# Optimization experiments

Hardware: AMD Instinct MI355X
Metric: run time of the kernel (lower is better)

The kernel has to match this reference:

```python
import jax, jax.numpy as jnp
import numpy as np


def setup_inputs() -> dict:
    key = jax.random.key(0)
    k1, k2, k3, k4 = jax.random.split(key, 4)
    B, T, C = 4, 1024, 768
    H, D = 12, 64
    scale = 0.02  # typical init scale for stability
    return {
        "x": jax.random.normal(k1, (B, T, C), dtype=jnp.float32),
        "Wq": jax.random.normal(k2, (H, C, D), dtype=jnp.float32) * scale,
        "Wk": jax.random.normal(k3, (H, C, D), dtype=jnp.float32) * scale,
        "Wv": jax.random.normal(k4, (H, C, D), dtype=jnp.float32) * scale,
    }


def reference(x, Wq, Wk, Wv):
    # x: [B,T,C]; Wq/Wk/Wv: [H,C,D]
    B, T, C = x.shape
    H, _, D = Wq.shape
    q = jnp.einsum("btc,hcd->bhtd", x, Wq)
    k = jnp.einsum("btc,hcd->bhtd", x, Wk)
    v = jnp.einsum("btc,hcd->bhtd", x, Wv)
    scores = jnp.einsum("bhtd,bhsd->bhts", q, k) * (D ** -0.5)
    causal = jnp.tril(jnp.ones((T, T), dtype=bool))
    scores = jnp.where(causal, scores, jnp.finfo(scores.dtype).min)
    attn = jax.nn.softmax(scores, axis=-1)
    out = jnp.einsum("bhts,bhsd->bhtd", attn, v)  # [B,H,T,D]
    # concat heads along last dim: [B,T,H*D]
    return out.transpose(0, 2, 1, 3).reshape(B, T, H * D)
```

## Files before the change

kernel.cpp:

```cpp
#include <hip/hip_runtime.h>
#include <math.h>
#include <stdint.h>

constexpr int B_ = 4, T_ = 1024, C_ = 768, H_ = 12, D_ = 64;
constexpr int BH_ = B_ * H_;
constexpr int M_ = B_ * T_;
constexpr int N_ = 3 * H_ * D_;

using f32x4 = __attribute__((ext_vector_type(4))) float;
using s16x8 = __attribute__((ext_vector_type(8))) short;

__device__ __forceinline__ unsigned short f2bf(float f) {
    union { float f; uint32_t u; } v; v.f = f;
    uint32_t u = v.u + 0x7fffu + ((v.u >> 16) & 1u);
    return (unsigned short)(u >> 16);
}

__global__ __launch_bounds__(256) void cast_x_kernel(
    const float* __restrict__ x, unsigned short* __restrict__ X16)
{
    int i = blockIdx.x * 256 + threadIdx.x;
    float4 v = ((const float4*)x)[i];
    ushort4 o;
    o.x = f2bf(v.x); o.y = f2bf(v.y); o.z = f2bf(v.z); o.w = f2bf(v.w);
    ((ushort4*)X16)[i] = o;
}

__global__ __launch_bounds__(256) void cast_w_kernel(
    const float* __restrict__ Wq, const float* __restrict__ Wk,
    const float* __restrict__ Wv, unsigned short* __restrict__ Wt)
{
    __shared__ unsigned short L[64][72];
    const int hp = blockIdx.x / 12, ct = blockIdx.x % 12;
    const int p = hp / H_, h = hp % H_;
    const float* W = (p == 0 ? Wq : (p == 1 ? Wk : Wv)) + (size_t)h * C_ * D_ + (size_t)ct * 64 * D_;
    const int tid = threadIdx.x;
#pragma unroll
    for (int it = 0; it < 4; ++it) {
        int f = tid + it * 256;
        int c = f >> 4, dg = f & 15;
        float4 v = ((const float4*)(W + (size_t)c * D_))[dg];
        L[dg * 4 + 0][c] = f2bf(v.x);
        L[dg * 4 + 1][c] = f2bf(v.y);
        L[dg * 4 + 2][c] = f2bf(v.z);
        L[dg * 4 + 3][c] = f2bf(v.w);
    }
    __syncthreads();
#pragma unroll
    for (int it = 0; it < 2; ++it) {
        int f = tid + it * 256;
        int d = f >> 3, cg = f & 7;
        uint4 v = *(const uint4*)&L[d][cg * 8];
        *(uint4*)(Wt + (size_t)(hp * 64 + d) * C_ + ct * 64 + cg * 8) = v;
    }
}

__global__ __launch_bounds__(256) void proj_kernel(
    const unsigned short* __restrict__ X16,
    const unsigned short* __restrict__ Wt,
    unsigned short* __restrict__ Qp,
    unsigned short* __restrict__ Kp,
    unsigned short* __restrict__ Vt)
{
    __shared__ unsigned short As[128 * 32];
    __shared__ unsigned short Bs[128 * 32];
    const int tid = threadIdx.x;
    const int l = tid & 63, w = tid >> 6;
    const int n0 = blockIdx.x * 128, m0 = blockIdx.y * 128;
    const int msub = (w >> 1) * 64, nsub = (w & 1) * 64;
    const int lr = l & 15, lg = l >> 4;

    f32x4 acc[4][4];
#pragma unroll
    for (int i = 0; i < 4; ++i)
#pragma unroll
        for (int j = 0; j < 4; ++j)
            acc[i][j] = (f32x4){0.f, 0.f, 0.f, 0.f};

    for (int k0 = 0; k0 < C_; k0 += 32) {
#pragma unroll
        for (int it = 0; it < 2; ++it) {
            int f = tid + it * 256;
            int m = f >> 2, kc = f & 3;
            uint4 va = *(const uint4*)(X16 + (size_t)(m0 + m) * C_ + k0 + kc * 8);
            *(uint4*)(As + f * 8) = va;
            uint4 vb = *(const uint4*)(Wt + (size_t)(n0 + m) * C_ + k0 + kc * 8);
            *(uint4*)(Bs + f * 8) = vb;
        }
        __syncthreads();
        s16x8 a[4], b[4];
#pragma unroll
        for (int i = 0; i < 4; ++i) {
            a[i] = *(const s16x8*)(As + (msub + i * 16 + lr) * 32 + lg * 8);
            b[i] = *(const s16x8*)(Bs + (nsub + i * 16 + lr) * 32 + lg * 8);
        }
#pragma unroll
        for (int i = 0; i < 4; ++i)
#pragma unroll
            for (int j = 0; j < 4; ++j)
                acc[i][j] = __builtin_amdgcn_mfma_f32_16x16x32_bf16(a[i], b[j], acc[i][j], 0, 0, 0);
        __syncthreads();
    }

    const int bq = m0 >> 10;
#pragma unroll
    for (int j = 0; j < 4; ++j) {
        int n = n0 + nsub + j * 16 + lr;
        int hp = n >> 6, d = n & 63;
        int p = hp / H_, hh = hp % H_;
        int bh = bq * H_ + hh;
#pragma unroll
        for (int i = 0; i < 4; ++i) {
            int tb = m0 + msub + i * 16 + lg * 4;
            int t = tb & (T_ - 1);
            if (p == 2) {
                ushort4 pv;
                pv.x = f2bf(acc[i][j][0]); pv.y = f2bf(acc[i][j][1]);
                pv.z = f2bf(acc[i][j][2]); pv.w = f2bf(acc[i][j][3]);
                *(ushort4*)(Vt + ((size_t)bh * D_ + d) * T_ + t) = pv;
            } else {
                unsigned short* P = (p == 0 ? Qp : Kp) + (size_t)bh * T_ * D_ + d;
#pragma unroll
                for (int r = 0; r < 4; ++r)
                    P[(size_t)(t + r) * D_] = f2bf(acc[i][j][r]);
            }
        }
    }
}

__global__ __launch_bounds__(64) void attn_kernel(
    const unsigned short* __restrict__ Qp,
    const unsigned short* __restrict__ Kp,
    const unsigned short* __restrict__ Vt,
    float* __restrict__ out)
{
    __shared__ unsigned short Pl[16 * 72];
    const int l = threadIdx.x;
    const int lr = l & 15, lg = l >> 4;
    const int bh = blockIdx.x >> 5, pr = blockIdx.x & 31;
    const int bq = bh / H_, hh = bh % H_;
    const unsigned short* Q = Qp + (size_t)bh * T_ * D_;
    const unsigned short* K = Kp + (size_t)bh * T_ * D_;
    const unsigned short* V = Vt + (size_t)bh * D_ * T_;
    float* O = out + (size_t)bq * T_ * (H_ * D_) + hh * D_;

    const float NEG = -30000.0f;

    for (int half = 0; half < 2; ++half) {
        const int qi = half ? (63 - pr) : pr;
        const int q0 = qi * 16;
        s16x8 qa0 = *(const s16x8*)(Q + (size_t)(q0 + lr) * D_ + lg * 8);
        s16x8 qa1 = *(const s16x8*)(Q + (size_t)(q0 + lr) * D_ + 32 + lg * 8);

        f32x4 o[4];
        float m[4], ll[4];
#pragma unroll
        for (int g = 0; g < 4; ++g) o[g] = (f32x4){0.f, 0.f, 0.f, 0.f};
#pragma unroll
        for (int r = 0; r < 4; ++r) { m[r] = NEG; ll[r] = 0.f; }

        const int ntile = (qi >> 2) + 1;
        for (int j = 0; j < ntile; ++j) {
            const int kv0 = j * 64;
            f32x4 s[4];
#pragma unroll
            for (int g = 0; g < 4; ++g) s[g] = (f32x4){0.f, 0.f, 0.f, 0.f};
#pragma unroll
            for (int g = 0; g < 4; ++g) {
                const unsigned short* kr = K + (size_t)(kv0 + g * 16 + lr) * D_ + lg * 8;
                s16x8 kb0 = *(const s16x8*)(kr);
                s16x8 kb1 = *(const s16x8*)(kr + 32);
                s[g] = __builtin_amdgcn_mfma_f32_16x16x32_bf16(qa0, kb0, s[g], 0, 0, 0);
                s[g] = __builtin_amdgcn_mfma_f32_16x16x32_bf16(qa1, kb1, s[g], 0, 0, 0);
            }
            const bool last = (j == ntile - 1);
            const float sc = 0.125f;
#pragma unroll
            for (int g = 0; g < 4; ++g)
#pragma unroll
                for (int r = 0; r < 4; ++r) {
                    float v = s[g][r] * sc;
                    if (last && (kv0 + g * 16 + lr > q0 + lg * 4 + r)) v = NEG;
                    s[g][r] = v;
                }
#pragma unroll
            for (int r = 0; r < 4; ++r) {
                float mx = fmaxf(fmaxf(s[0][r], s[1][r]), fmaxf(s[2][r], s[3][r]));
                mx = fmaxf(mx, __shfl_xor(mx, 1));
                mx = fmaxf(mx, __shfl_xor(mx, 2));
                mx = fmaxf(mx, __shfl_xor(mx, 4));
                mx = fmaxf(mx, __shfl_xor(mx, 8));
                float mn = fmaxf(m[r], mx);
                float corr = __expf(m[r] - mn);
                float p[4], rs = 0.f;
#pragma unroll
                for (int g = 0; g < 4; ++g) { p[g] = __expf(s[g][r] - mn); rs += p[g]; }
                rs += __shfl_xor(rs, 1); rs += __shfl_xor(rs, 2);
                rs += __shfl_xor(rs, 4); rs += __shfl_xor(rs, 8);
                ll[r] = ll[r] * corr + rs;
                m[r] = mn;
#pragma unroll
                for (int g = 0; g < 4; ++g) {
                    o[g][r] *= corr;
                    Pl[(lg * 4 + r) * 72 + g * 16 + lr] = f2bf(p[g]);
                }
            }
            __syncthreads();

            s16x8 pa0 = *(const s16x8*)(Pl + lr * 72 + lg * 8);
            s16x8 pa1 = *(const s16x8*)(Pl + lr * 72 + 32 + lg * 8);
#pragma unroll
            for (int g = 0; g < 4; ++g) {
                const unsigned short* vr = V + (size_t)(g * 16 + lr) * T_ + kv0 + lg * 8;
                s16x8 vb0 = *(const s16x8*)(vr);
                s16x8 vb1 = *(const s16x8*)(vr + 32);
                o[g] = __builtin_amdgcn_mfma_f32_16x16x32_bf16(pa0, vb0, o[g], 0, 0, 0);
                o[g] = __builtin_amdgcn_mfma_f32_16x16x32_bf16(pa1, vb1, o[g], 0, 0, 0);
            }
            __syncthreads();
        }
        float rinv[4];
#pragma unroll
        for (int r = 0; r < 4; ++r) rinv[r] = 1.0f / ll[r];
#pragma unroll
        for (int g = 0; g < 4; ++g)
#pragma unroll
            for (int r = 0; r < 4; ++r)
                O[(size_t)(q0 + lg * 4 + r) * (H_ * D_) + g * 16 + lr] = o[g][r] * rinv[r];
    }
}

extern "C" void kernel_launch(void* const* d_in, const int* in_sizes, int n_in,
                              void* d_out, int out_size, void* d_ws, size_t ws_size,
                              hipStream_t stream) {
    const float* x  = (const float*)d_in[0];
    const float* Wq = (const float*)d_in[1];
    const float* Wk = (const float*)d_in[2];
    const float* Wv = (const float*)d_in[3];
    float* out = (float*)d_out;

    char* ws = (char*)d_ws;
    unsigned short* X16 = (unsigned short*)(ws);
    unsigned short* Wt  = (unsigned short*)(ws + 6291456);
    unsigned short* Qp  = (unsigned short*)(ws + 9830400);
    unsigned short* Kp  = (unsigned short*)(ws + 16121856);
    unsigned short* Vt  = (unsigned short*)(ws + 22413312);

    cast_x_kernel<<<(M_ * C_ / 4) / 256, 256, 0, stream>>>(x, X16);
    cast_w_kernel<<<36 * 12, 256, 0, stream>>>(Wq, Wk, Wv, Wt);
    proj_kernel<<<dim3(N_ / 128, M_ / 128), 256, 0, stream>>>(X16, Wt, Qp, Kp, Vt);
    attn_kernel<<<BH_ * 32, 64, 0, stream>>>(Qp, Kp, Vt, out);
}
```

Measured before the change: 183.4 us.

## Split attention blocks per query tile, map heads to XCDs, prefetch K and V

Each attention block now handles a single 16-row query tile instead of a balanced pair, doubling the grid to 3072 single-wave blocks. Block indices are remapped so that all query tiles of one batch-head land on the same XCD, which should improve L2 reuse of K and V. V tiles are loaded together with K before the QK MFMAs, hiding V latency behind the softmax. A launch-bounds occupancy hint is added. The change gives up the paired load balancing, so causal work per block is now uneven, and holding 16 extra vector registers for K and V may limit occupancy.

```diff
diff --git a/kernel.cpp b/kernel.cpp
--- a/kernel.cpp
+++ b/kernel.cpp
@@ -128,7 +128,7 @@
     }
 }
 
-__global__ __launch_bounds__(64) void attn_kernel(
+__global__ __launch_bounds__(64, 3) void attn_kernel(
     const unsigned short* __restrict__ Qp,
     const unsigned short* __restrict__ Kp,
     const unsigned short* __restrict__ Vt,
@@ -137,7 +137,10 @@
     __shared__ unsigned short Pl[16 * 72];
     const int l = threadIdx.x;
     const int lr = l & 15, lg = l >> 4;
-    const int bh = blockIdx.x >> 5, pr = blockIdx.x & 31;
+    const int id = blockIdx.x;
+    const int xcd = id & 7, rest = id >> 3;
+    const int qi = rest & 63;
+    const int bh = xcd + 8 * (rest >> 6);
     const int bq = bh / H_, hh = bh % H_;
     const unsigned short* Q = Qp + (size_t)bh * T_ * D_;
     const unsigned short* K = Kp + (size_t)bh * T_ * D_;
@@ -145,89 +148,94 @@
     float* O = out + (size_t)bq * T_ * (H_ * D_) + hh * D_;
 
     const float NEG = -30000.0f;
-
-    for (int half = 0; half < 2; ++half) {
-        const int qi = half ? (63 - pr) : pr;
-        const int q0 = qi * 16;
-        s16x8 qa0 = *(const s16x8*)(Q + (size_t)(q0 + lr) * D_ + lg * 8);
-        s16x8 qa1 = *(const s16x8*)(Q + (size_t)(q0 + lr) * D_ + 32 + lg * 8);
-
-        f32x4 o[4];
-        float m[4], ll[4];
-#pragma unroll
-        for (int g = 0; g < 4; ++g) o[g] = (f32x4){0.f, 0.f, 0.f, 0.f};
-#pragma unroll
-        for (int r = 0; r < 4; ++r) { m[r] = NEG; ll[r] = 0.f; }
-
-        const int ntile = (qi >> 2) + 1;
-        for (int j = 0; j < ntile; ++j) {
-            const int kv0 = j * 64;
-            f32x4 s[4];
-#pragma unroll
-            for (int g = 0; g < 4; ++g) s[g] = (f32x4){0.f, 0.f, 0.f, 0.f};
+    const int q0 = qi * 16;
+
+    s16x8 qa0 = *(const s16x8*)(Q + (size_t)(q0 + lr) * D_ + lg * 8);
+    s16x8 qa1 = *(const s16x8*)(Q + (size_t)(q0 + lr) * D_ + 32 + lg * 8);
+
+    f32x4 o[4];
+    float m[4], ll[4];
+#pragma unroll
+    for (int g = 0; g < 4; ++g) o[g] = (f32x4){0.f, 0.f, 0.f, 0.f};
+#pragma unroll
+    for (int r = 0; r < 4; ++r) { m[r] = NEG; ll[r] = 0.f; }
+
+    const int ntile = (qi >> 2) + 1;
+    for (int j = 0; j < ntile; ++j) {
+        const int kv0 = j * 64;
+        s16x8 kb[8], vb[8];
+#pragma unroll
+        for (int g = 0; g < 4; ++g) {
+            const unsigned short* kr = K + (size_t)(kv0 + g * 16 + lr) * D_ + lg * 8;
+            kb[2 * g]     = *(const s16x8*)(kr);
+            kb[2 * g + 1] = *(const s16x8*)(kr + 32);
+        }
+#pragma unroll
+        for (int g = 0; g < 4; ++g) {
+            const unsigned short* vr = V + (size_t)(g * 16 + lr) * T_ + kv0 + lg * 8;
+            vb[2 * g]     = *(const s16x8*)(vr);
+            vb[2 * g + 1] = *(const s16x8*)(vr + 32);
+        }
+        f32x4 s[4];
+#pragma unroll
+        for (int g = 0; g < 4; ++g) s[g] = (f32x4){0.f, 0.f, 0.f, 0.f};
+#pragma unroll
+        for (int g = 0; g < 4; ++g) {
+            s[g] = __builtin_amdgcn_mfma_f32_16x16x32_bf16(qa0, kb[2 * g],     s[g], 0, 0, 0);
+            s[g] = __builtin_amdgcn_mfma_f32_16x16x32_bf16(qa1, kb[2 * g + 1], s[g], 0, 0, 0);
+        }
+        const bool last = (j == ntile - 1);
+        const float sc = 0.125f;
+#pragma unroll
+        for (int g = 0; g < 4; ++g)
+#pragma unroll
+            for (int r = 0; r < 4; ++r) {
+                float v = s[g][r] * sc;
+                if (last && (kv0 + g * 16 + lr > q0 + lg * 4 + r)) v = NEG;
+                s[g][r] = v;
+            }
+#pragma unroll
+        for (int r = 0; r < 4; ++r) {
+            float mx = fmaxf(fmaxf(s[0][r], s[1][r]), fmaxf(s[2][r], s[3][r]));
+            mx = fmaxf(mx, __shfl_xor(mx, 1));
+            mx = fmaxf(mx, __shfl_xor(mx, 2));
+            mx = fmaxf(mx, __shfl_xor(mx, 4));
+            mx = fmaxf(mx, __shfl_xor(mx, 8));
+            float mn = fmaxf(m[r], mx);
+            float corr = __expf(m[r] - mn);
+            float p[4], rs = 0.f;
+#pragma unroll
+            for (int g = 0; g < 4; ++g) { p[g] = __expf(s[g][r] - mn); rs += p[g]; }
+            rs += __shfl_xor(rs, 1); rs += __shfl_xor(rs, 2);
+            rs += __shfl_xor(rs, 4); rs += __shfl_xor(rs, 8);
+            ll[r] = ll[r] * corr + rs;
+            m[r] = mn;
 #pragma unroll
             for (int g = 0; g < 4; ++g) {
-                const unsigned short* kr = K + (size_t)(kv0 + g * 16 + lr) * D_ + lg * 8;
-                s16x8 kb0 = *(const s16x8*)(kr);
-                s16x8 kb1 = *(const s16x8*)(kr + 32);
-                s[g] = __builtin_amdgcn_mfma_f32_16x16x32_bf16(qa0, kb0, s[g], 0, 0, 0);
-                s[g] = __builtin_amdgcn_mfma_f32_16x16x32_bf16(qa1, kb1, s[g], 0, 0, 0);
+                o[g][r] *= corr;
+                Pl[(lg * 4 + r) * 72 + g * 16 + lr] = f2bf(p[g]);
             }
-            const bool last = (j == ntile - 1);
-            const float sc = 0.125f;
-#pragma unroll
-            for (int g = 0; g < 4; ++g)
-#pragma unroll
-                for (int r = 0; r < 4; ++r) {
-                    float v = s[g][r] * sc;
-                    if (last && (kv0 + g * 16 + lr > q0 + lg * 4 + r)) v = NEG;
-                    s[g][r] = v;
-                }
-#pragma unroll
-            for (int r = 0; r < 4; ++r) {
-                float mx = fmaxf(fmaxf(s[0][r], s[1][r]), fmaxf(s[2][r], s[3][r]));
-                mx = fmaxf(mx, __shfl_xor(mx, 1));
-                mx = fmaxf(mx, __shfl_xor(mx, 2));
-                mx = fmaxf(mx, __shfl_xor(mx, 4));
-                mx = fmaxf(mx, __shfl_xor(mx, 8));
-                float mn = fmaxf(m[r], mx);
-                float corr = __expf(m[r] - mn);
-                float p[4], rs = 0.f;
-#pragma unroll
-                for (int g = 0; g < 4; ++g) { p[g] = __expf(s[g][r] - mn); rs += p[g]; }
-                rs += __shfl_xor(rs, 1); rs += __shfl_xor(rs, 2);
-                rs += __shfl_xor(rs, 4); rs += __shfl_xor(rs, 8);
-                ll[r] = ll[r] * corr + rs;
-                m[r] = mn;
-#pragma unroll
-                for (int g = 0; g < 4; ++g) {
-                    o[g][r] *= corr;
-                    Pl[(lg * 4 + r) * 72 + g * 16 + lr] = f2bf(p[g]);
-                }
-            }
-            __syncthreads();
-
-            s16x8 pa0 = *(const s16x8*)(Pl + lr * 72 + lg * 8);
-            s16x8 pa1 = *(const s16x8*)(Pl + lr * 72 + 32 + lg * 8);
-#pragma unroll
-            for (int g = 0; g < 4; ++g) {
-                const unsigned short* vr = V + (size_t)(g * 16 + lr) * T_ + kv0 + lg * 8;
-                s16x8 vb0 = *(const s16x8*)(vr);
-                s16x8 vb1 = *(const s16x8*)(vr + 32);
-                o[g] = __builtin_amdgcn_mfma_f32_16x16x32_bf16(pa0, vb0, o[g], 0, 0, 0);
-                o[g] = __builtin_amdgcn_mfma_f32_16x16x32_bf16(pa1, vb1, o[g], 0, 0, 0);
-            }
-            __syncthreads();
-        }
-        float rinv[4];
-#pragma unroll
-        for (int r = 0; r < 4; ++r) rinv[r] = 1.0f / ll[r];
-#pragma unroll
-        for (int g = 0; g < 4; ++g)
-#pragma unroll
-            for (int r = 0; r < 4; ++r)
-                O[(size_t)(q0 + lg * 4 + r) * (H_ * D_) + g * 16 + lr] = o[g][r] * rinv[r];
-    }
+        }
+        __syncthreads();
+
+        s16x8 pa0 = *(const s16x8*)(Pl + lr * 72 + lg * 8);
+        s16x8 pa1 = *(const s16x8*)(Pl + lr * 72 + 32 + lg * 8);
+#pragma unroll
+        for (int g = 0; g < 4; ++g) {
+            o[g] = __builtin_amdgcn_mfma_f32_16x16x32_bf16(pa0, vb[2 * g],     o[g], 0, 0, 0);
+            o[g] = __builtin_amdgcn_mfma_f32_16x16x32_bf16(pa1, vb[2 * g + 1], o[g], 0, 0, 0);
+        }
+        __syncthreads();
+    }
+
+    float rinv[4];
+#pragma unroll
+    for (int r = 0; r < 4; ++r) rinv[r] = 1.0f / ll[r];
+#pragma unroll
+    for (int g = 0; g < 4; ++g)
+#pragma unroll
+        for (int r = 0; r < 4; ++r)
+            O[(size_t)(q0 + lg * 4 + r) * (H_ * D_) + g * 16 + lr] = o[g][r] * rinv[r];
 }
 
 extern "C" void kernel_launch(void* const* d_in, const int* in_sizes, int n_in,
@@ -249,5 +257,5 @@
     cast_x_kernel<<<(M_ * C_ / 4) / 256, 256, 0, stream>>>(x, X16);
     cast_w_kernel<<<36 * 12, 256, 0, stream>>>(Wq, Wk, Wv, Wt);
     proj_kernel<<<dim3(N_ / 128, M_ / 128), 256, 0, stream>>>(X16, Wt, Qp, Kp, Vt);
-    attn_kernel<<<BH_ * 32, 64, 0, stream>>>(Qp, Kp, Vt, out);
-}
+    attn_kernel<<<BH_ * 64, 64, 0, stream>>>(Qp, Kp, Vt, out);
+}
```

After: 182.7 us. About the same (-0.4%).
